# Kernel tuning notes

Hardware: AMD Instinct MI355X
Metric: run time of the kernel (lower is better)

The kernel has to match this reference:

```python
import jax, jax.numpy as jnp
import numpy as np
from math import factorial, sqrt, pi

# ---- static config (matches init_kwargs) ----
C = 64            # channel multiplicity of hidden irreps 64x0e+64x1o+64x2e
L_HID = 2
MAX_ELL = 3
N_BASIS = 8
R_MAX = 5.0
AVG_NEI = 16.0
NUM_SPECIES = 5
N_NODES = 10000
N_EDGES = 160000
RAD_HID = 64
DIMS = [2 * l + 1 for l in range(L_HID + 1)]   # [1,3,5]

# ---- Clebsch-Gordan coefficients in the real spherical-harmonic basis ----
def _cg(j1, m1, j2, m2, j3, m3):
    if m1 + m2 != m3:
        return 0.0
    f = factorial
    pref = sqrt((2 * j3 + 1) * f(j3 + j1 - j2) * f(j3 - j1 + j2) * f(j1 + j2 - j3) / f(j1 + j2 + j3 + 1))
    pref *= sqrt(f(j3 + m3) * f(j3 - m3) * f(j1 - m1) * f(j1 + m1) * f(j2 - m2) * f(j2 + m2))
    s = 0.0
    for k in range(j1 + j2 - j3 + 1):
        d = (k, j1 + j2 - j3 - k, j1 - m1 - k, j2 + m2 - k, j3 - j2 + m1 + k, j3 - j1 - m2 + k)
        if min(d) < 0:
            continue
        s += (-1.0) ** k / np.prod([float(f(x)) for x in d])
    return pref * s

def _real_basis(l):
    A = np.zeros((2 * l + 1, 2 * l + 1), dtype=complex)
    for mp in range(-l, l + 1):
        if mp > 0:
            A[l + mp, l + mp] = (-1) ** mp / sqrt(2); A[l + mp, l - mp] = 1 / sqrt(2)
        elif mp == 0:
            A[l, l] = 1.0
        else:
            m = -mp
            A[l + mp, l - m] = 1j / sqrt(2); A[l + mp, l + m] = -1j * (-1) ** m / sqrt(2)
    return A

def _real_cg(l1, l2, l3):
    Cc = np.zeros((2 * l1 + 1, 2 * l2 + 1, 2 * l3 + 1), dtype=complex)
    for a in range(-l1, l1 + 1):
        for b in range(-l2, l2 + 1):
            c = a + b
            if -l3 <= c <= l3:
                Cc[l1 + a, l2 + b, l3 + c] = _cg(l1, a, l2, b, l3, c)
    A1, A2, A3 = _real_basis(l1), _real_basis(l2), _real_basis(l3)
    Cr = np.einsum('ia,jb,kc,abc->ijk', A1, A2, A3.conj(), Cc)
    R = Cr.real if np.abs(Cr.real).sum() >= np.abs(Cr.imag).sum() else Cr.imag
    R = R / max(np.sqrt((R ** 2).sum()), 1e-12)   # path-normalized
    return jnp.asarray(R.astype(np.float32))

def _paths(ls_in):
    ps = []
    for l1 in ls_in:
        for l2 in range(MAX_ELL + 1):
            for l3 in range(L_HID + 1):
                # triangle inequality + parity match (hidden parities are (-1)^l, SH parity (-1)^l)
                if abs(l1 - l2) <= l3 <= l1 + l2 and (l1 + l2 + l3) % 2 == 0:
                    ps.append((l1, l2, l3))
    return ps

PATHS = [_paths([0]), _paths(list(range(L_HID + 1)))]   # layer 0: 3 paths, layer 1: 13 paths
CG = {p: _real_cg(*p) for layer in PATHS for p in layer}

# ---- real spherical harmonics up to l=3 (component-style normalization) ----
def sph_harm(u):
    x, y, z = u[:, 0], u[:, 1], u[:, 2]
    Y0 = jnp.ones_like(x)[:, None]
    Y1 = sqrt(3.0) * jnp.stack([y, z, x], -1)
    Y2 = jnp.stack([sqrt(15) * x * y, sqrt(15) * y * z, sqrt(5) / 2 * (3 * z * z - 1),
                    sqrt(15) * x * z, sqrt(15) / 2 * (x * x - y * y)], -1)
    Y3 = jnp.stack([sqrt(35 / 8) * y * (3 * x * x - y * y), sqrt(105) * x * y * z,
                    sqrt(21 / 8) * y * (5 * z * z - 1), sqrt(7) / 2 * z * (5 * z * z - 3),
                    sqrt(21 / 8) * x * (5 * z * z - 1), sqrt(105) / 2 * z * (x * x - y * y),
                    sqrt(35 / 8) * x * (x * x - 3 * y * y)], -1)
    return [Y0, Y1, Y2, Y3]

def bessel(r):
    # e3nn.bessel(r, N_BASIS, R_MAX)
    n = jnp.arange(1, N_BASIS + 1, dtype=r.dtype)
    rs = jnp.maximum(r, 1e-6)[:, None]
    return sqrt(2.0 / R_MAX) * jnp.sin(n * pi * rs / R_MAX) / rs

def soft_envelope(r):
    # e3nn.soft_envelope: value_at_origin=1.2, arg_multiplicator=2.0
    t = 2.0 * (1.0 - r / R_MAX)
    sus = jnp.where(t > 0, jnp.exp(-1.0 / jnp.where(t > 0, t, 1.0)), 0.0)
    return (1.2 / np.exp(-0.5)) * sus

def interaction(h, Ys, rad, paths, rad_w1, rad_w2, mix, senders, receivers, n_nodes):
    # radial MLP -> per-path, per-channel tensor-product weights
    w = jax.nn.silu(rad @ rad_w1) @ rad_w2                       # [E, P*C]
    w = w.reshape(rad.shape[0], len(paths), C)
    hs = {l: h[l][senders] for l in {p[0] for p in paths}}       # gather once per input l
    acc = [None] * (L_HID + 1)
    for p, (l1, l2, l3) in enumerate(paths):
        # CG tensor product of sender features with edge spherical harmonics
        m = jnp.einsum('eci,ej,ijk,ec->eck', hs[l1], Ys[l2], CG[(l1, l2, l3)], w[:, p])
        acc[l3] = m if acc[l3] is None else acc[l3] + m
    out = {}
    for l in range(L_HID + 1):
        node_m = jax.ops.segment_sum(acc[l], receivers, num_segments=n_nodes) / AVG_NEI
        out[l] = jnp.einsum('nck,cd->ndk', node_m, mix[l])       # linear channel mixing per irrep
    return out

def forward(positions, w_embed, rad_w1_0, rad_w2_0, mix0, read0,
            rad_w1_1, rad_w2_1, mix1, skip1, read1, species, senders, receivers):
    n = positions.shape[0]
    rel = positions[receivers] - positions[senders]              # [E,3]
    r = jnp.sqrt(jnp.sum(rel * rel, -1) + 1e-12)
    u = rel / r[:, None]
    Ys = sph_harm(u)
    rad = bessel(r) * soft_envelope(r)[:, None]                  # [E,B]
    h = {0: w_embed[species][:, :, None]}                        # initial scalar node features
    # layer 0 (skip_connection_first_layer=False)
    h = interaction(h, Ys, rad, PATHS[0], rad_w1_0, rad_w2_0, mix0, senders, receivers, n)
    out0 = jnp.concatenate([jnp.einsum('nck,cd->ndk', h[l], read0[l]).reshape(n, -1)
                            for l in range(L_HID + 1)], -1)      # [N, C*9]
    # layer 1 (with linear skip connection)
    m = interaction(h, Ys, rad, PATHS[1], rad_w1_1, rad_w2_1, mix1, senders, receivers, n)
    h = {l: m[l] + jnp.einsum('nck,cd->ndk', h[l], skip1[l]) for l in range(L_HID + 1)}
    out1 = jnp.concatenate([jnp.einsum('nck,cd->ndk', h[l], read1[l]).reshape(n, -1)
                            for l in range(L_HID + 1)], -1)
    # per-layer readouts stacked then flattened == axis_to_mul over the layer axis
    return jnp.concatenate([out0, out1], -1)                     # [N, 2*C*9] = [N, 1152]

def setup_inputs() -> dict:
    key = jax.random.key(0)
    ks = jax.random.split(key, 14)
    P = [len(PATHS[0]), len(PATHS[1])]
    def w(k, shape, fan_in):
        return jax.random.normal(k, shape, jnp.float32) / np.sqrt(fan_in)
    return {
        'positions': jax.random.normal(ks[0], (N_NODES, 3), jnp.float32) * 1.5,
        'species': jax.random.randint(ks[1], (N_NODES,), 0, NUM_SPECIES),
        'senders': jax.random.randint(ks[2], (N_EDGES,), 0, N_NODES),
        'receivers': jax.random.randint(ks[3], (N_EDGES,), 0, N_NODES),
        'w_embed': w(ks[4], (NUM_SPECIES, C), 1),
        'rad_w1_0': w(ks[5], (N_BASIS, RAD_HID), N_BASIS),
        'rad_w2_0': w(ks[6], (RAD_HID, P[0] * C), RAD_HID),
        'mix0': w(ks[7], (L_HID + 1, C, C), C),
        'read0': w(ks[8], (L_HID + 1, C, C), C),
        'rad_w1_1': w(ks[9], (N_BASIS, RAD_HID), N_BASIS),
        'rad_w2_1': w(ks[10], (RAD_HID, P[1] * C), RAD_HID),
        'mix1': w(ks[11], (L_HID + 1, C, C), C),
        'skip1': w(ks[12], (L_HID + 1, C, C), C),
        'read1': w(ks[13], (L_HID + 1, C, C), C),
    }

def reference(positions, species, senders, receivers, w_embed, rad_w1_0, rad_w2_0, mix0, read0,
              rad_w1_1, rad_w2_1, mix1, skip1, read1):
    return forward(positions, w_embed, rad_w1_0, rad_w2_0, mix0, read0,
                   rad_w1_1, rad_w2_1, mix1, skip1, read1, species, senders, receivers)
```

## Files before the change

### kernel.cpp

```cpp
#include <hip/hip_runtime.h>
#include <math.h>

#define NE 160000
#define NN 10000
#define NP1 13
#define CG_TOTAL 573
#define CC_TOTAL 171
#define G_TOTAL 145

typedef __attribute__((ext_vector_type(8))) short bf16x8;
typedef __attribute__((ext_vector_type(4))) float f32x4;

constexpr int c_l1[NP1]   = {0,0,0,1,1,1,1,1,2,2,2,2,2};
constexpr int c_l2[NP1]   = {0,1,2,0,1,1,2,3,0,1,2,2,3};
constexpr int c_l3[NP1]   = {0,1,2,1,0,2,1,2,2,1,0,2,1};
constexpr int c_cgoff[NP1+1]= {0,1,10,35,44,53,98,143,248,273,318,343,468,573};
constexpr int c_ccoff[NP1+1]= {0,1,4,9,12,21,30,45,66,71,86,111,136,171};
constexpr int c_goff[NP1] = {0,1,4,9,18,21,36,45,60,85,100,105,130};
constexpr int YB[4] = {0,1,4,9};
constexpr int KB[3] = {0,1,4};
constexpr int IB[3] = {0,1,4};

__device__ float g_cg[640];
__device__ int   g_dec[160];
__device__ float g_ys[(size_t)NE*16];
__device__ float g_rad[(size_t)NE*8];
__device__ unsigned short g_hb0[(size_t)NE*64];
__device__ unsigned short g_hb1[(size_t)NE*64];
__device__ unsigned short g_Bp0[12*2*64*8];
__device__ unsigned short g_Bp1[52*2*64*8];
__device__ unsigned short g_W0[(size_t)NE*192];
__device__ unsigned short g_W1[(size_t)NE*832];
__device__ float g_acc0[(size_t)NN*576];
__device__ float g_acc1[(size_t)NN*576];
__device__ float g_h0[(size_t)NN*576];
__device__ int g_cnt[NN];
__device__ int g_cur[NN];
__device__ int g_off[NN+1];
__device__ int g_perm[NE];

__device__ inline unsigned short f2bf(float f){
  unsigned u = __float_as_uint(f);
  unsigned r = (u + 0x7FFFu + ((u>>16)&1u)) >> 16;
  return (unsigned short)r;
}
__device__ inline float bf2f(unsigned short h){ return __uint_as_float(((unsigned)h)<<16); }
__device__ inline float silu(float a){ return a/(1.f+expf(-a)); }

__device__ double dfact(int n){ double f=1.0; for(int i=2;i<=n;++i) f*=(double)i; return f; }

__device__ double cg_coef(int j1,int m1,int j2,int m2,int j3,int m3){
  if(m1+m2!=m3) return 0.0;
  double pref = sqrt((2.0*j3+1.0)*dfact(j3+j1-j2)*dfact(j3-j1+j2)*dfact(j1+j2-j3)/dfact(j1+j2+j3+1));
  pref *= sqrt(dfact(j3+m3)*dfact(j3-m3)*dfact(j1-m1)*dfact(j1+m1)*dfact(j2-m2)*dfact(j2+m2));
  double s=0.0;
  for(int k=0;k<=j1+j2-j3;++k){
    int d0=k, d1=j1+j2-j3-k, d2=j1-m1-k, d3=j2+m2-k, d4=j3-j2+m1+k, d5=j3-j1-m2+k;
    if(d1<0||d2<0||d3<0||d4<0||d5<0) continue;
    double denom = dfact(d0)*dfact(d1)*dfact(d2)*dfact(d3)*dfact(d4)*dfact(d5);
    s += ((k&1)? -1.0:1.0)/denom;
  }
  return pref*s;
}

__device__ inline void rb_elem(int l, int i, int j, double& re, double& im){
  re=0.0; im=0.0;
  int mp = i - l;
  const double is2 = 0.70710678118654752440;
  if(mp>0){
    if(j==l+mp) re = ((mp&1)? -1.0:1.0)*is2;
    else if(j==l-mp) re = is2;
  } else if(mp==0){
    if(j==l) re = 1.0;
  } else {
    int m=-mp;
    if(j==l-m) im = is2;
    else if(j==l+m) im = -(((m&1)?-1.0:1.0))*is2;
  }
}

__global__ __launch_bounds__(1024) void k_cg(){
  __shared__ double s_cc[CC_TOTAL];
  __shared__ double s_crr[CG_TOTAL];
  __shared__ double s_cri[CG_TOTAL];
  __shared__ double s_inv[NP1];
  __shared__ int    s_useR[NP1];
  int tid = threadIdx.x;

  if(tid==0){
    int r=0;
    for(int q=0;q<NP1;q++){
      int l1=c_l1[q], l2=c_l2[q], l3=c_l3[q];
      int d1=2*l1+1, d2=2*l2+1, d3=2*l3+1;
      for(int i=0;i<d1;i++)for(int k=0;k<d3;k++){
        int cgs = c_cgoff[q] + i*d2*d3 + k;
        g_dec[r++] = cgs | (YB[l2]<<10) | (d2<<14) | (d3<<17);
      }
    }
  }

  if(tid < CC_TOTAL){
    int p=0; while(tid >= c_ccoff[p+1]) p++;
    int r = tid - c_ccoff[p];
    int l1=c_l1[p], l2=c_l2[p], l3=c_l3[p];
    int d2=2*l2+1;
    int ai = r/d2, bi = r - ai*d2;
    int a = ai - l1, b = bi - l2, c = a + b;
    double v = 0.0;
    if(c >= -l3 && c <= l3) v = cg_coef(l1,a,l2,b,l3,c);
    s_cc[tid] = v;
  }
  __syncthreads();

  if(tid < CG_TOTAL){
    int p=0; while(tid >= c_cgoff[p+1]) p++;
    int r = tid - c_cgoff[p];
    int l1=c_l1[p], l2=c_l2[p], l3=c_l3[p];
    int d2=2*l2+1, d3=2*l3+1;
    int i = r/(d2*d3), rem = r - i*(d2*d3);
    int j = rem/d3, k = rem - j*d3;
    double accr=0.0, acci=0.0;
    int d1=2*l1+1;
    for(int ai=0; ai<d1; ai++){
      double a1r,a1i; rb_elem(l1,i,ai,a1r,a1i);
      if(a1r==0.0 && a1i==0.0) continue;
      for(int bi=0; bi<d2; bi++){
        double cc = s_cc[c_ccoff[p] + ai*d2 + bi];
        if(cc==0.0) continue;
        int ci = (ai - l1) + (bi - l2) + l3;
// ... 30 lines not shown
    double v = s_useR[p]? s_crr[tid] : s_cri[tid];
    g_cg[tid] = (float)(v*s_inv[p]);
  }
}

__global__ void k_zero(){
  int i = blockIdx.x*256 + threadIdx.x;
  if(i<NN){ g_cnt[i]=0; g_cur[i]=0; }
}

__global__ void k_hist(const int* __restrict__ rcv){
  int e = blockIdx.x*256 + threadIdx.x;
  if(e<NE) atomicAdd(&g_cnt[rcv[e]], 1);
}

__global__ void k_scan(){
  __shared__ int lds[1024];
  int t = threadIdx.x;
  int base = t*10;
  int s = 0;
  for(int i=0;i<10;i++){ int idx=base+i; if(idx<NN) s += g_cnt[idx]; }
  lds[t]=s; __syncthreads();
  for(int o=1;o<1024;o<<=1){
    int v = (t>=o)? lds[t-o] : 0;
    __syncthreads();
    lds[t]+=v;
    __syncthreads();
  }
  int run = lds[t]-s;
  for(int i=0;i<10;i++){ int idx=base+i; if(idx<NN){ g_off[idx]=run; run+=g_cnt[idx]; } }
  if(t==0) g_off[NN]=NE;
}

__global__ void k_scatter(const int* __restrict__ rcv){
  int e = blockIdx.x*256 + threadIdx.x;
  if(e<NE){
    int r = rcv[e];
    int p = atomicAdd(&g_cur[r],1);
    g_perm[g_off[r]+p] = e;
  }
}

__global__ void k_edge(const float* __restrict__ pos, const int* __restrict__ snd,
                       const int* __restrict__ rcv){
  int e = blockIdx.x*blockDim.x + threadIdx.x;
  if(e>=NE) return;
  int s=snd[e], r=rcv[e];
  float dx=pos[r*3+0]-pos[s*3+0];
  float dy=pos[r*3+1]-pos[s*3+1];
  float dz=pos[r*3+2]-pos[s*3+2];
  float rr = sqrtf(dx*dx+dy*dy+dz*dz + 1e-12f);
  float x=dx/rr, y=dy/rr, z=dz/rr;
  float* Y=&g_ys[(size_t)e*16];
  Y[0]=1.f;
  const float s3=1.7320508075688772f;
  Y[1]=s3*y; Y[2]=s3*z; Y[3]=s3*x;
  const float s15=3.872983346207417f;
  const float s5h=1.118033988749895f;
  Y[4]=s15*x*y; Y[5]=s15*y*z; Y[6]=s5h*(3.f*z*z-1.f); Y[7]=s15*x*z; Y[8]=0.5f*s15*(x*x-y*y);
  const float s35_8=2.0916500663351889f;
  const float s105=10.246950765959598f;
  const float s21_8=1.6201851746019651f;
  const float s7h=1.3228756555322954f;
  Y[9]=s35_8*y*(3.f*x*x-y*y);
  Y[10]=s105*x*y*z;
  Y[11]=s21_8*y*(5.f*z*z-1.f);
  Y[12]=s7h*z*(5.f*z*z-3.f);
  Y[13]=s21_8*x*(5.f*z*z-1.f);
  Y[14]=0.5f*s105*z*(x*x-y*y);
  Y[15]=s35_8*x*(x*x-3.f*y*y);
  float t = 2.f*(1.f - rr*0.2f);
  float env = (t>0.f)? 1.9784655248401538f*expf(-1.f/t) : 0.f;
  float rs = fmaxf(rr,1e-6f);
  const float sq25 = 0.6324555320336759f;
  float pre = sq25/rs * env;
  const float pi5 = 0.6283185307179586f;
  #pragma unroll
  for(int b=0;b<8;b++){
    g_rad[(size_t)e*8+b] = pre * sinf((float)(b+1)*pi5*rs);
  }
}

__global__ __launch_bounds__(256) void k_hidden(const float* __restrict__ W1a,
                                                const float* __restrict__ W1b){
  int idx = blockIdx.x*256 + threadIdx.x;
  int c = idx & 63;
  const float* rd = &g_rad[(size_t)(idx>>6)*8];
  float a0=0.f, a1=0.f;
  #pragma unroll
  for(int b=0;b<8;b++){
    float rv = rd[b];
    a0 += rv*W1a[b*64+c];
    a1 += rv*W1b[b*64+c];
  }
  g_hb0[idx] = f2bf(silu(a0));
  g_hb1[idx] = f2bf(silu(a1));
}

template<int NCOLS>
__global__ void k_repack(const float* __restrict__ W2){
  constexpr int NCB = NCOLS/16;
  int t = blockIdx.x*256 + threadIdx.x;
  if(t >= NCB*128) return;
  int cb = t>>7, rest = t&127, ks = rest>>6, l = rest&63;
  int col = cb*16 + (l&15);
  unsigned short* dst = (NCOLS==832)? g_Bp1 : g_Bp0;
  #pragma unroll
  for(int j=0;j<8;j++){
    int k = ks*32 + ((l>>4)<<3) + j;
    dst[(size_t)t*8+j] = f2bf(W2[k*NCOLS + col]);
  }
}

template<int NCOLS>
__global__ __launch_bounds__(256) void k_wgemm(){
  constexpr int NCB = NCOLS/16;
  const unsigned short* hb = (NCOLS==832)? g_hb1 : g_hb0;
  const unsigned short* Bp = (NCOLS==832)? g_Bp1 : g_Bp0;
  unsigned short* W = (NCOLS==832)? g_W1 : g_W0;
  const int lane = threadIdx.x & 63;
  const int wid  = threadIdx.x >> 6;
  const int e0 = blockIdx.x*128 + wid*32;
  const int rowl = lane & 15, kg = lane >> 4;
  bf16x8 a[2][2];
  #pragma unroll
  for(int mr=0;mr<2;mr++){
    #pragma unroll
    for(int ks=0;ks<2;ks++){
      a[mr][ks] = *reinterpret_cast<const bf16x8*>(&hb[(size_t)(e0+mr*16+rowl)*64 + ks*32 + kg*8]);
    }
  }
  for(int cb=0;cb<NCB;cb++){
    bf16x8 b0 = *reinterpret_cast<const bf16x8*>(&Bp[((size_t)(cb*2+0)*64+lane)*8]);
    bf16x8 b1 = *reinterpret_cast<const bf16x8*>(&Bp[((size_t)(cb*2+1)*64+lane)*8]);
    #pragma unroll
    for(int mr=0;mr<2;mr++){
      f32x4 acc = {0.f,0.f,0.f,0.f};
      acc = __builtin_amdgcn_mfma_f32_16x16x32_bf16(a[mr][0], b0, acc, 0,0,0);
      acc = __builtin_amdgcn_mfma_f32_16x16x32_bf16(a[mr][1], b1, acc, 0,0,0);
      #pragma unroll
      for(int r=0;r<4;r++){
        int row = kg*4 + r;
        W[(size_t)(e0+mr*16+row)*NCOLS + cb*16 + rowl] = f2bf(acc[r]);
      }
    }
  }
}

__global__ __launch_bounds__(256) void k_gather0(const int* __restrict__ snd,
    const int* __restrict__ spec, const float* __restrict__ wemb){
  __shared__ float lds_cg[36];
  __shared__ int lds_dec[9];
  __shared__ float Ylds[4][16];
  __shared__ float Glds[4][12];
  int tid=threadIdx.x;
  if(tid<36) lds_cg[tid]=g_cg[tid];
  if(tid>=64 && tid<73) lds_dec[tid-64]=g_dec[tid-64];
  __syncthreads();
  int lane=tid&63, wid=tid>>6;
  int n = blockIdx.x*4 + wid;
  int beg=g_off[n], end=g_off[n+1];
  float acc[9];
  #pragma unroll
  for(int kk=0;kk<9;kk++) acc[kk]=0.f;
  for(int j=beg;j<end;j++){
    int e = __builtin_amdgcn_readfirstlane(g_perm[j]);
    int s = __builtin_amdgcn_readfirstlane(snd[e]);
    if(lane<16) Ylds[wid][lane]=g_ys[(size_t)e*16+lane];
    const unsigned short* wp=&g_W0[(size_t)e*192 + lane];
    float wv0=bf2f(wp[0]), wv1=bf2f(wp[64]), wv2=bf2f(wp[128]);
    float hs=wemb[spec[s]*64+lane];
    asm volatile("s_waitcnt lgkmcnt(0)" ::: "memory");
    if(lane<9){
      int d=lds_dec[lane];
      int cgs=d&1023, yb=(d>>10)&15, d2=(d>>14)&7, d3=(d>>17)&7;
      float g=0.f;
      for(int jj=0;jj<d2;jj++) g+=Ylds[wid][yb+jj]*lds_cg[cgs+jj*d3];
      Glds[wid][lane]=g;
    }
    asm volatile("s_waitcnt lgkmcnt(0)" ::: "memory");
    float whs0=wv0*hs, whs1=wv1*hs, whs2=wv2*hs;
    acc[0]+=whs0*Glds[wid][0];
    #pragma unroll
    for(int k=0;k<3;k++) acc[1+k]+=whs1*Glds[wid][1+k];
    #pragma unroll
    for(int k=0;k<5;k++) acc[4+k]+=whs2*Glds[wid][4+k];
    asm volatile("s_waitcnt lgkmcnt(0)" ::: "memory");
  }
  #pragma unroll
  for(int kk=0;kk<9;kk++) g_acc0[(size_t)n*576+kk*64+lane]=acc[kk];
}

__global__ __launch_bounds__(256) void k_gather1(const int* __restrict__ snd){
  __shared__ float lds_cg[CG_TOTAL];
  __shared__ int lds_dec[G_TOTAL];
  __shared__ float Ylds[4][16];
  __shared__ float Glds[4][152];
  int tid=threadIdx.x;
  for(int t=tid;t<CG_TOTAL;t+=256) lds_cg[t]=g_cg[t];
  for(int t=tid;t<G_TOTAL;t+=256) lds_dec[t]=g_dec[t];
  __syncthreads();
  int lane=tid&63, wid=tid>>6;
  int n = blockIdx.x*4 + wid;
  int beg=g_off[n], end=g_off[n+1];
  float acc[9];
  #pragma unroll
  for(int kk=0;kk<9;kk++) acc[kk]=0.f;
  for(int j=beg;j<end;j++){
    int e = __builtin_amdgcn_readfirstlane(g_perm[j]);
    int s = __builtin_amdgcn_readfirstlane(snd[e]);
    if(lane<16) Ylds[wid][lane]=g_ys[(size_t)e*16+lane];
    float wv[13];
    const unsigned short* wp=&g_W1[(size_t)e*832 + lane];
    #pragma unroll
    for(int p=0;p<13;p++) wv[p]=bf2f(wp[p*64]);
    const float* hb=&g_h0[(size_t)s*576 + lane];
    float hsv[9];
    #pragma unroll
    for(int i=0;i<9;i++) hsv[i]=hb[i*64];
    asm volatile("s_waitcnt lgkmcnt(0)" ::: "memory");
    #pragma unroll
    for(int strip=0;strip<3;strip++){
      int r = lane + strip*64;
      if(r<G_TOTAL){
        int d=lds_dec[r];
        int cgs=d&1023, yb=(d>>10)&15, d2=(d>>14)&7, d3=(d>>17)&7;
        float g=0.f;
        for(int jj=0;jj<d2;jj++) g+=Ylds[wid][yb+jj]*lds_cg[cgs+jj*d3];
        Glds[wid][r]=g;
      }
    }
    asm volatile("s_waitcnt lgkmcnt(0)" ::: "memory");
    const float* G=&Glds[wid][0];
    #pragma unroll
    for(int p=0;p<13;p++){
      const int l1=c_l1[p], l3=c_l3[p];
      const int d1=2*l1+1, d3=2*l3+1;
      const int ib=IB[l1], kb=KB[l3], go=c_goff[p];
      float wpv=wv[p];
      #pragma unroll
      for(int k=0;k<d3;k++){
        float t=0.f;
        #pragma unroll
        for(int i=0;i<d1;i++) t += hsv[ib+i]*G[go+i*d3+k];
        acc[kb+k] += wpv*t;
      }
    }
    asm volatile("s_waitcnt lgkmcnt(0)" ::: "memory");
  }
  #pragma unroll
  for(int kk=0;kk<9;kk++) g_acc1[(size_t)n*576+kk*64+lane]=acc[kk];
}

__global__ __launch_bounds__(256) void k_node0(const float* __restrict__ mix,
    const float* __restrict__ read, float* __restrict__ out){
  __shared__ float nm[4][9][64];
  __shared__ float hl[4][9][64];
  int lane=threadIdx.x&63, wid=threadIdx.x>>6;
  int n=blockIdx.x*4+wid;
  #pragma unroll
  for(int kk=0;kk<9;kk++) nm[wid][kk][lane]=g_acc0[(size_t)n*576+kk*64+lane]*(1.f/16.f);
  asm volatile("s_waitcnt lgkmcnt(0)" ::: "memory");
  float h[9];
  #pragma unroll
  for(int kk=0;kk<9;kk++) h[kk]=0.f;
  for(int c=0;c<64;c++){
    float m0=mix[c*64+lane], m1=mix[4096+c*64+lane], m2=mix[8192+c*64+lane];
    h[0]+=nm[wid][0][c]*m0;
    #pragma unroll
    for(int k=0;k<3;k++) h[1+k]+=nm[wid][1+k][c]*m1;
    #pragma unroll
    for(int k=0;k<5;k++) h[4+k]+=nm[wid][4+k][c]*m2;
  }
  #pragma unroll
  for(int kk=0;kk<9;kk++){ g_h0[(size_t)n*576+kk*64+lane]=h[kk]; hl[wid][kk][lane]=h[kk]; }
  asm volatile("s_waitcnt lgkmcnt(0)" ::: "memory");
  float o[9];
  #pragma unroll
  for(int kk=0;kk<9;kk++) o[kk]=0.f;
  for(int c=0;c<64;c++){
    float r0=read[c*64+lane], r1=read[4096+c*64+lane], r2=read[8192+c*64+lane];
    o[0]+=hl[wid][0][c]*r0;
    #pragma unroll
    for(int k=0;k<3;k++) o[1+k]+=hl[wid][1+k][c]*r1;
// ... 47 lines not shown
    #pragma unroll
    for(int k=0;k<5;k++) o[4+k]+=hn[wid][4+k][c]*r2;
  }
  float* op=&out[(size_t)n*1152 + 576];
  op[lane]=o[0];
  #pragma unroll
  for(int k=0;k<3;k++) op[64 + lane*3+k]=o[1+k];
  #pragma unroll
  for(int k=0;k<5;k++) op[256 + lane*5+k]=o[4+k];
}

extern "C" void kernel_launch(void* const* d_in, const int* in_sizes, int n_in,
                              void* d_out, int out_size, void* d_ws, size_t ws_size,
                              hipStream_t stream) {
  (void)in_sizes; (void)n_in; (void)out_size; (void)d_ws; (void)ws_size;
  const float* pos  =(const float*)d_in[0];
  const int*   spec =(const int*)  d_in[1];
  const int*   snd  =(const int*)  d_in[2];
  const int*   rcv  =(const int*)  d_in[3];
  const float* wemb =(const float*)d_in[4];
  const float* w1_0 =(const float*)d_in[5];
  const float* w2_0 =(const float*)d_in[6];
  const float* mix0 =(const float*)d_in[7];
  const float* read0=(const float*)d_in[8];
  const float* w1_1 =(const float*)d_in[9];
  const float* w2_1 =(const float*)d_in[10];
  const float* mix1 =(const float*)d_in[11];
  const float* skip1=(const float*)d_in[12];
  const float* read1=(const float*)d_in[13];
  float* out=(float*)d_out;

  k_cg<<<1,1024,0,stream>>>();
  k_zero<<<(NN+255)/256,256,0,stream>>>();
  k_edge<<<(NE+255)/256,256,0,stream>>>(pos,snd,rcv);
  k_hist<<<NE/256,256,0,stream>>>(rcv);
  k_scan<<<1,1024,0,stream>>>();
  k_scatter<<<NE/256,256,0,stream>>>(rcv);
  k_hidden<<<NE*64/256,256,0,stream>>>(w1_0,w1_1);
  k_repack<192><<<6,256,0,stream>>>(w2_0);
  k_repack<832><<<26,256,0,stream>>>(w2_1);
  k_wgemm<192><<<NE/128,256,0,stream>>>();
  k_wgemm<832><<<NE/128,256,0,stream>>>();
  k_gather0<<<NN/4,256,0,stream>>>(snd,spec,wemb);
  k_node0<<<NN/4,256,0,stream>>>(mix0,read0,out);
  k_gather1<<<NN/4,256,0,stream>>>(snd);
  k_node1<<<NN/4,256,0,stream>>>(mix1,skip1,read1,out);
}
```

Baseline: 670.3 us.

## Fuse radial weight GEMM into receiver-sorted gather kernels using MFMA per 16-edge tile

Drops the separate per-edge weight GEMM kernels and their large bf16 weight buffers, and computes the radial weights with MFMA inside the gather kernels, 16 receiver-sorted edges at a time. Edge features, radial basis, sender ids and species are written in receiver-sorted order, so the gather reads contiguous rows and no permutation lookup is needed. This removes a large write and re-read of the edge weight tensors and processes edges in tiles instead of one by one. The cost is heavier per-wave register and LDS use, plus partial-tile handling and a shuffle reduction at the end.

```diff
diff --git a/kernel.cpp b/kernel.cpp
--- a/kernel.cpp
+++ b/kernel.cpp
@@ -29,22 +29,21 @@
 __device__ unsigned short g_hb1[(size_t)NE*64];
 __device__ unsigned short g_Bp0[12*2*64*8];
 __device__ unsigned short g_Bp1[52*2*64*8];
-__device__ unsigned short g_W0[(size_t)NE*192];
-__device__ unsigned short g_W1[(size_t)NE*832];
 __device__ float g_acc0[(size_t)NN*576];
 __device__ float g_acc1[(size_t)NN*576];
 __device__ float g_h0[(size_t)NN*576];
 __device__ int g_cnt[NN];
 __device__ int g_cur[NN];
 __device__ int g_off[NN+1];
-__device__ int g_perm[NE];
+__device__ int g_jof[NE];
+__device__ int g_snds[NE];
+__device__ int g_specs[NE];
 
 __device__ inline unsigned short f2bf(float f){
   unsigned u = __float_as_uint(f);
   unsigned r = (u + 0x7FFFu + ((u>>16)&1u)) >> 16;
   return (unsigned short)r;
 }
-__device__ inline float bf2f(unsigned short h){ return __uint_as_float(((unsigned)h)<<16); }
 __device__ inline float silu(float a){ return a/(1.f+expf(-a)); }
 
 __device__ double dfact(int n){ double f=1.0; for(int i=2;i<=n;++i) f*=(double)i; return f; }
@@ -191,12 +190,17 @@
   if(t==0) g_off[NN]=NE;
 }
 
-__global__ void k_scatter(const int* __restrict__ rcv){
+__global__ void k_scatter(const int* __restrict__ rcv, const int* __restrict__ snd,
+                          const int* __restrict__ spec){
   int e = blockIdx.x*256 + threadIdx.x;
   if(e<NE){
     int r = rcv[e];
     int p = atomicAdd(&g_cur[r],1);
-    g_perm[g_off[r]+p] = e;
+    int j = g_off[r]+p;
+    g_jof[e] = j;
+    int s = snd[e];
+    g_snds[j] = s;
+    g_specs[j] = spec[s];
   }
 }
 
@@ -205,12 +209,13 @@
   int e = blockIdx.x*blockDim.x + threadIdx.x;
   if(e>=NE) return;
   int s=snd[e], r=rcv[e];
+  int j=g_jof[e];
   float dx=pos[r*3+0]-pos[s*3+0];
   float dy=pos[r*3+1]-pos[s*3+1];
   float dz=pos[r*3+2]-pos[s*3+2];
   float rr = sqrtf(dx*dx+dy*dy+dz*dz + 1e-12f);
   float x=dx/rr, y=dy/rr, z=dz/rr;
-  float* Y=&g_ys[(size_t)e*16];
+  float Y[16];
   Y[0]=1.f;
   const float s3=1.7320508075688772f;
   Y[1]=s3*y; Y[2]=s3*z; Y[3]=s3*x;
@@ -228,6 +233,8 @@
   Y[13]=s21_8*x*(5.f*z*z-1.f);
   Y[14]=0.5f*s105*z*(x*x-y*y);
   Y[15]=s35_8*x*(x*x-3.f*y*y);
+  #pragma unroll
+  for(int i=0;i<16;i++) g_ys[(size_t)j*16+i]=Y[i];
   float t = 2.f*(1.f - rr*0.2f);
   float env = (t>0.f)? 1.9784655248401538f*expf(-1.f/t) : 0.f;
   float rs = fmaxf(rr,1e-6f);
@@ -236,7 +243,7 @@
   const float pi5 = 0.6283185307179586f;
   #pragma unroll
   for(int b=0;b<8;b++){
-    g_rad[(size_t)e*8+b] = pre * sinf((float)(b+1)*pi5*rs);
+    g_rad[(size_t)j*8+b] = pre * sinf((float)(b+1)*pi5*rs);
   }
 }
 
@@ -271,144 +278,190 @@
   }
 }
 
-template<int NCOLS>
-__global__ __launch_bounds__(256) void k_wgemm(){
-  constexpr int NCB = NCOLS/16;
-  const unsigned short* hb = (NCOLS==832)? g_hb1 : g_hb0;
-  const unsigned short* Bp = (NCOLS==832)? g_Bp1 : g_Bp0;
-  unsigned short* W = (NCOLS==832)? g_W1 : g_W0;
-  const int lane = threadIdx.x & 63;
-  const int wid  = threadIdx.x >> 6;
-  const int e0 = blockIdx.x*128 + wid*32;
-  const int rowl = lane & 15, kg = lane >> 4;
-  bf16x8 a[2][2];
-  #pragma unroll
-  for(int mr=0;mr<2;mr++){
-    #pragma unroll
-    for(int ks=0;ks<2;ks++){
-      a[mr][ks] = *reinterpret_cast<const bf16x8*>(&hb[(size_t)(e0+mr*16+rowl)*64 + ks*32 + kg*8]);
-    }
-  }
-  for(int cb=0;cb<NCB;cb++){
-    bf16x8 b0 = *reinterpret_cast<const bf16x8*>(&Bp[((size_t)(cb*2+0)*64+lane)*8]);
-    bf16x8 b1 = *reinterpret_cast<const bf16x8*>(&Bp[((size_t)(cb*2+1)*64+lane)*8]);
-    #pragma unroll
-    for(int mr=0;mr<2;mr++){
-      f32x4 acc = {0.f,0.f,0.f,0.f};
-      acc = __builtin_amdgcn_mfma_f32_16x16x32_bf16(a[mr][0], b0, acc, 0,0,0);
-      acc = __builtin_amdgcn_mfma_f32_16x16x32_bf16(a[mr][1], b1, acc, 0,0,0);
-      #pragma unroll
-      for(int r=0;r<4;r++){
-        int row = kg*4 + r;
-        W[(size_t)(e0+mr*16+row)*NCOLS + cb*16 + rowl] = f2bf(acc[r]);
-      }
-    }
-  }
-}
-
-__global__ __launch_bounds__(256) void k_gather0(const int* __restrict__ snd,
-    const int* __restrict__ spec, const float* __restrict__ wemb){
+__global__ __launch_bounds__(256) void k_gfuse0(const float* __restrict__ wemb){
   __shared__ float lds_cg[36];
   __shared__ int lds_dec[9];
-  __shared__ float Ylds[4][16];
-  __shared__ float Glds[4][12];
+  __shared__ float Ylds[4][16][16];
+  __shared__ float Glds[4][16][12];
+  __shared__ int Slds[4][16];
   int tid=threadIdx.x;
   if(tid<36) lds_cg[tid]=g_cg[tid];
   if(tid>=64 && tid<73) lds_dec[tid-64]=g_dec[tid-64];
   __syncthreads();
-  int lane=tid&63, wid=tid>>6;
-  int n = blockIdx.x*4 + wid;
-  int beg=g_off[n], end=g_off[n+1];
-  float acc[9];
-  #pragma unroll
-  for(int kk=0;kk<9;kk++) acc[kk]=0.f;
-  for(int j=beg;j<end;j++){
-    int e = __builtin_amdgcn_readfirstlane(g_perm[j]);
-    int s = __builtin_amdgcn_readfirstlane(snd[e]);
-    if(lane<16) Ylds[wid][lane]=g_ys[(size_t)e*16+lane];
-    const unsigned short* wp=&g_W0[(size_t)e*192 + lane];
-    float wv0=bf2f(wp[0]), wv1=bf2f(wp[64]), wv2=bf2f(wp[128]);
-    float hs=wemb[spec[s]*64+lane];
+  const int lane=tid&63, wid=tid>>6;
+  const int sub=lane&15, kg=lane>>4;
+  const int n=blockIdx.x*4+wid;
+  const int beg=g_off[n], end=g_off[n+1];
+  float acc[4][9];
+  #pragma unroll
+  for(int q=0;q<4;q++)
+    #pragma unroll
+    for(int k=0;k<9;k++) acc[q][k]=0.f;
+  for(int j0=beg;j0<end;j0+=16){
+    const int nrow = min(16,end-j0);
+    for(int t=lane;t<256;t+=64){
+      int r=t>>4, c2=t&15;
+      int j=j0+r; if(j>end-1) j=end-1;
+      Ylds[wid][r][c2]=g_ys[(size_t)j*16+c2];
+    }
+    if(lane<16){ int j=j0+lane; Slds[wid][lane]=(j<end)? g_specs[j] : 0; }
     asm volatile("s_waitcnt lgkmcnt(0)" ::: "memory");
-    if(lane<9){
-      int d=lds_dec[lane];
-      int cgs=d&1023, yb=(d>>10)&15, d2=(d>>14)&7, d3=(d>>17)&7;
-      float g=0.f;
-      for(int jj=0;jj<d2;jj++) g+=Ylds[wid][yb+jj]*lds_cg[cgs+jj*d3];
-      Glds[wid][lane]=g;
-    }
+    for(int t=lane;t<144;t+=64){
+      int r=t/9, g=t-r*9;
+      float gv=0.f;
+      if(r<nrow){
+        int d=lds_dec[g];
+        int cgs=d&1023, yb=(d>>10)&15, d2=(d>>14)&7, d3=(d>>17)&7;
+        for(int jj=0;jj<d2;jj++) gv+=Ylds[wid][r][yb+jj]*lds_cg[cgs+jj*d3];
+      }
+      Glds[wid][r][g]=gv;
+    }
+    size_t arow=(size_t)(j0+sub); if(arow>(size_t)(NE-1)) arow=NE-1;
+    bf16x8 a0=*reinterpret_cast<const bf16x8*>(&g_hb0[arow*64 + kg*8]);
+    bf16x8 a1=*reinterpret_cast<const bf16x8*>(&g_hb0[arow*64 + 32 + kg*8]);
     asm volatile("s_waitcnt lgkmcnt(0)" ::: "memory");
-    float whs0=wv0*hs, whs1=wv1*hs, whs2=wv2*hs;
-    acc[0]+=whs0*Glds[wid][0];
-    #pragma unroll
-    for(int k=0;k<3;k++) acc[1+k]+=whs1*Glds[wid][1+k];
-    #pragma unroll
-    for(int k=0;k<5;k++) acc[4+k]+=whs2*Glds[wid][4+k];
+    #pragma unroll
+    for(int cq=0;cq<4;cq++){
+      const int c=cq*16+sub;
+      float hv[4];
+      #pragma unroll
+      for(int r2=0;r2<4;r2++) hv[r2]=wemb[Slds[wid][kg*4+r2]*64+c];
+      #pragma unroll
+      for(int p=0;p<3;p++){
+        const int cb=p*4+cq;
+        bf16x8 b0=*reinterpret_cast<const bf16x8*>(&g_Bp0[((size_t)(cb*2+0)*64+lane)*8]);
+        bf16x8 b1=*reinterpret_cast<const bf16x8*>(&g_Bp0[((size_t)(cb*2+1)*64+lane)*8]);
+        f32x4 wv={0.f,0.f,0.f,0.f};
+        wv=__builtin_amdgcn_mfma_f32_16x16x32_bf16(a0,b0,wv,0,0,0);
+        wv=__builtin_amdgcn_mfma_f32_16x16x32_bf16(a1,b1,wv,0,0,0);
+        const int d3=2*p+1, kb=KB[p], go=(p==0)?0:((p==1)?1:4);
+        #pragma unroll
+        for(int r2=0;r2<4;r2++){
+          const int row=kg*4+r2;
+          float whp=wv[r2]*hv[r2];
+          #pragma unroll
+          for(int k=0;k<d3;k++) acc[cq][kb+k]+=whp*Glds[wid][row][go+k];
+        }
+      }
+    }
     asm volatile("s_waitcnt lgkmcnt(0)" ::: "memory");
   }
   #pragma unroll
-  for(int kk=0;kk<9;kk++) g_acc0[(size_t)n*576+kk*64+lane]=acc[kk];
-}
-
-__global__ __launch_bounds__(256) void k_gather1(const int* __restrict__ snd){
+  for(int q=0;q<4;q++)
+    #pragma unroll
+    for(int k=0;k<9;k++){
+      float v=acc[q][k];
+      v+=__shfl_xor(v,16,64);
+      v+=__shfl_xor(v,32,64);
+      acc[q][k]=v;
+    }
+  const int c=kg*16+sub;
+  #pragma unroll
+  for(int k=0;k<9;k++){
+    float v=acc[0][k];
+    if(kg==1) v=acc[1][k];
+    if(kg==2) v=acc[2][k];
+    if(kg==3) v=acc[3][k];
+    g_acc0[(size_t)n*576 + k*64 + c]=v;
+  }
+}
+
+__global__ __launch_bounds__(256) void k_gfuse1(){
   __shared__ float lds_cg[CG_TOTAL];
   __shared__ int lds_dec[G_TOTAL];
-  __shared__ float Ylds[4][16];
-  __shared__ float Glds[4][152];
+  __shared__ float Ylds[4][16][16];
+  __shared__ float Glds[4][16][148];
   int tid=threadIdx.x;
   for(int t=tid;t<CG_TOTAL;t+=256) lds_cg[t]=g_cg[t];
   for(int t=tid;t<G_TOTAL;t+=256) lds_dec[t]=g_dec[t];
   __syncthreads();
-  int lane=tid&63, wid=tid>>6;
-  int n = blockIdx.x*4 + wid;
-  int beg=g_off[n], end=g_off[n+1];
-  float acc[9];
-  #pragma unroll
-  for(int kk=0;kk<9;kk++) acc[kk]=0.f;
-  for(int j=beg;j<end;j++){
-    int e = __builtin_amdgcn_readfirstlane(g_perm[j]);
-    int s = __builtin_amdgcn_readfirstlane(snd[e]);
-    if(lane<16) Ylds[wid][lane]=g_ys[(size_t)e*16+lane];
-    float wv[13];
-    const unsigned short* wp=&g_W1[(size_t)e*832 + lane];
-    #pragma unroll
-    for(int p=0;p<13;p++) wv[p]=bf2f(wp[p*64]);
-    const float* hb=&g_h0[(size_t)s*576 + lane];
-    float hsv[9];
-    #pragma unroll
-    for(int i=0;i<9;i++) hsv[i]=hb[i*64];
+  const int lane=tid&63, wid=tid>>6;
+  const int sub=lane&15, kg=lane>>4;
+  const int n=blockIdx.x*4+wid;
+  const int beg=g_off[n], end=g_off[n+1];
+  float acc[4][9];
+  #pragma unroll
+  for(int q=0;q<4;q++)
+    #pragma unroll
+    for(int k=0;k<9;k++) acc[q][k]=0.f;
+  for(int j0=beg;j0<end;j0+=16){
+    const int nrow = min(16,end-j0);
+    for(int t=lane;t<256;t+=64){
+      int r=t>>4, c2=t&15;
+      int j=j0+r; if(j>end-1) j=end-1;
+      Ylds[wid][r][c2]=g_ys[(size_t)j*16+c2];
+    }
     asm volatile("s_waitcnt lgkmcnt(0)" ::: "memory");
-    #pragma unroll
-    for(int strip=0;strip<3;strip++){
-      int r = lane + strip*64;
-      if(r<G_TOTAL){
-        int d=lds_dec[r];
+    for(int t=lane;t<16*G_TOTAL;t+=64){
+      int r=t/G_TOTAL, g=t-r*G_TOTAL;
+      float gv=0.f;
+      if(r<nrow){
+        int d=lds_dec[g];
         int cgs=d&1023, yb=(d>>10)&15, d2=(d>>14)&7, d3=(d>>17)&7;
-        float g=0.f;
-        for(int jj=0;jj<d2;jj++) g+=Ylds[wid][yb+jj]*lds_cg[cgs+jj*d3];
-        Glds[wid][r]=g;
+        for(int jj=0;jj<d2;jj++) gv+=Ylds[wid][r][yb+jj]*lds_cg[cgs+jj*d3];
       }
-    }
+      Glds[wid][r][g]=gv;
+    }
+    size_t arow=(size_t)(j0+sub); if(arow>(size_t)(NE-1)) arow=NE-1;
+    bf16x8 a0=*reinterpret_cast<const bf16x8*>(&g_hb1[arow*64 + kg*8]);
+    bf16x8 a1=*reinterpret_cast<const bf16x8*>(&g_hb1[arow*64 + 32 + kg*8]);
+    int sv[4];
+    #pragma unroll
+    for(int r2=0;r2<4;r2++){ int j=j0+kg*4+r2; sv[r2]=(j<end)? g_snds[j] : 0; }
     asm volatile("s_waitcnt lgkmcnt(0)" ::: "memory");
-    const float* G=&Glds[wid][0];
-    #pragma unroll
-    for(int p=0;p<13;p++){
-      const int l1=c_l1[p], l3=c_l3[p];
-      const int d1=2*l1+1, d3=2*l3+1;
-      const int ib=IB[l1], kb=KB[l3], go=c_goff[p];
-      float wpv=wv[p];
+    #pragma unroll
+    for(int cq=0;cq<4;cq++){
+      const int c=cq*16+sub;
+      float h0v[4][9];
       #pragma unroll
-      for(int k=0;k<d3;k++){
-        float t=0.f;
+      for(int r2=0;r2<4;r2++)
         #pragma unroll
-        for(int i=0;i<d1;i++) t += hsv[ib+i]*G[go+i*d3+k];
-        acc[kb+k] += wpv*t;
+        for(int i=0;i<9;i++) h0v[r2][i]=g_h0[(size_t)sv[r2]*576 + i*64 + c];
+      #pragma unroll
+      for(int p=0;p<13;p++){
+        const int cb=p*4+cq;
+        bf16x8 b0=*reinterpret_cast<const bf16x8*>(&g_Bp1[((size_t)(cb*2+0)*64+lane)*8]);
+        bf16x8 b1=*reinterpret_cast<const bf16x8*>(&g_Bp1[((size_t)(cb*2+1)*64+lane)*8]);
+        f32x4 wv={0.f,0.f,0.f,0.f};
+        wv=__builtin_amdgcn_mfma_f32_16x16x32_bf16(a0,b0,wv,0,0,0);
+        wv=__builtin_amdgcn_mfma_f32_16x16x32_bf16(a1,b1,wv,0,0,0);
+        const int l1=c_l1[p], l3=c_l3[p];
+        const int d1=2*l1+1, d3=2*l3+1;
+        const int ib=IB[l1], kb=KB[l3], go=c_goff[p];
+        #pragma unroll
+        for(int r2=0;r2<4;r2++){
+          const int row=kg*4+r2;
+          float wp=wv[r2];
+          #pragma unroll
+          for(int k=0;k<d3;k++){
+            float t=0.f;
+            #pragma unroll
+            for(int i=0;i<d1;i++) t+=h0v[r2][ib+i]*Glds[wid][row][go+i*d3+k];
+            acc[cq][kb+k]+=wp*t;
+          }
+        }
       }
     }
     asm volatile("s_waitcnt lgkmcnt(0)" ::: "memory");
   }
   #pragma unroll
-  for(int kk=0;kk<9;kk++) g_acc1[(size_t)n*576+kk*64+lane]=acc[kk];
+  for(int q=0;q<4;q++)
+    #pragma unroll
+    for(int k=0;k<9;k++){
+      float v=acc[q][k];
+      v+=__shfl_xor(v,16,64);
+      v+=__shfl_xor(v,32,64);
+      acc[q][k]=v;
+    }
+  const int c=kg*16+sub;
+  #pragma unroll
+  for(int k=0;k<9;k++){
+    float v=acc[0][k];
+    if(kg==1) v=acc[1][k];
+    if(kg==2) v=acc[2][k];
+    if(kg==3) v=acc[3][k];
+    g_acc1[(size_t)n*576 + k*64 + c]=v;
+  }
 }
 
 __global__ __launch_bounds__(256) void k_node0(const float* __restrict__ mix,
@@ -522,17 +575,15 @@
 
   k_cg<<<1,1024,0,stream>>>();
   k_zero<<<(NN+255)/256,256,0,stream>>>();
-  k_edge<<<(NE+255)/256,256,0,stream>>>(pos,snd,rcv);
   k_hist<<<NE/256,256,0,stream>>>(rcv);
   k_scan<<<1,1024,0,stream>>>();
-  k_scatter<<<NE/256,256,0,stream>>>(rcv);
+  k_scatter<<<NE/256,256,0,stream>>>(rcv,snd,spec);
+  k_edge<<<(NE+255)/256,256,0,stream>>>(pos,snd,rcv);
   k_hidden<<<NE*64/256,256,0,stream>>>(w1_0,w1_1);
   k_repack<192><<<6,256,0,stream>>>(w2_0);
   k_repack<832><<<26,256,0,stream>>>(w2_1);
-  k_wgemm<192><<<NE/128,256,0,stream>>>();
-  k_wgemm<832><<<NE/128,256,0,stream>>>();
-  k_gather0<<<NN/4,256,0,stream>>>(snd,spec,wemb);
+  k_gfuse0<<<NN/4,256,0,stream>>>(wemb);
   k_node0<<<NN/4,256,0,stream>>>(mix0,read0,out);
-  k_gather1<<<NN/4,256,0,stream>>>(snd);
+  k_gfuse1<<<NN/4,256,0,stream>>>();
   k_node1<<<NN/4,256,0,stream>>>(mix1,skip1,read1,out);
 }
```

Result: slower. 2.439 ms (+263.9%).

## Store edge data in receiver-sorted order and precompute Y·CG per edge

Applied to the files above, without the earlier changes.

Edge features, spherical harmonics and radial bases are now written in receiver-sorted order, so the gather kernels read contiguous rows instead of going through a permutation. A new kernel precomputes the CG-contracted Y products per edge into padded global buffers, and the gather kernels load them as vector loads instead of recomputing them per edge in LDS with waits. This removes indirection and per-edge LDS work from the gathers, at the cost of extra global storage and traffic (about 172 floats per edge) plus another kernel launch.

```diff
diff --git a/kernel.cpp b/kernel.cpp
--- a/kernel.cpp
+++ b/kernel.cpp
@@ -7,6 +7,8 @@
 #define CG_TOTAL 573
 #define CC_TOTAL 171
 #define G_TOTAL 145
+#define G1PAD 172
+#define G0PAD 16
 
 typedef __attribute__((ext_vector_type(8))) short bf16x8;
 typedef __attribute__((ext_vector_type(4))) float f32x4;
@@ -16,13 +18,13 @@
 constexpr int c_l3[NP1]   = {0,1,2,1,0,2,1,2,2,1,0,2,1};
 constexpr int c_cgoff[NP1+1]= {0,1,10,35,44,53,98,143,248,273,318,343,468,573};
 constexpr int c_ccoff[NP1+1]= {0,1,4,9,12,21,30,45,66,71,86,111,136,171};
-constexpr int c_goff[NP1] = {0,1,4,9,18,21,36,45,60,85,100,105,130};
+constexpr int c_poff1[NP1] = {0,4,8,16,28,32,48,60,76,104,120,128,156};
+constexpr int c_poff0[3]   = {0,4,8};
 constexpr int YB[4] = {0,1,4,9};
-constexpr int KB[3] = {0,1,4};
-constexpr int IB[3] = {0,1,4};
 
 __device__ float g_cg[640];
-__device__ int   g_dec[160];
+__device__ int   g_dec1[160];
+__device__ int   g_dec0[16];
 __device__ float g_ys[(size_t)NE*16];
 __device__ float g_rad[(size_t)NE*8];
 __device__ unsigned short g_hb0[(size_t)NE*64];
@@ -31,13 +33,17 @@
 __device__ unsigned short g_Bp1[52*2*64*8];
 __device__ unsigned short g_W0[(size_t)NE*192];
 __device__ unsigned short g_W1[(size_t)NE*832];
+__device__ float g_G1[(size_t)NE*G1PAD];
+__device__ float g_G0[(size_t)NE*G0PAD];
 __device__ float g_acc0[(size_t)NN*576];
 __device__ float g_acc1[(size_t)NN*576];
 __device__ float g_h0[(size_t)NN*576];
 __device__ int g_cnt[NN];
 __device__ int g_cur[NN];
 __device__ int g_off[NN+1];
-__device__ int g_perm[NE];
+__device__ int g_jof[NE];
+__device__ int g_snds[NE];
+__device__ int g_specs[NE];
 
 __device__ inline unsigned short f2bf(float f){
   unsigned u = __float_as_uint(f);
@@ -90,11 +96,22 @@
   if(tid==0){
     int r=0;
     for(int q=0;q<NP1;q++){
-      int l1=c_l1[q], l2=c_l2[q], l3=c_l3[q];
-      int d1=2*l1+1, d2=2*l2+1, d3=2*l3+1;
+      int l2=c_l2[q], l3=c_l3[q];
+      int d1=2*c_l1[q]+1, d2=2*l2+1, d3=2*l3+1;
       for(int i=0;i<d1;i++)for(int k=0;k<d3;k++){
         int cgs = c_cgoff[q] + i*d2*d3 + k;
-        g_dec[r++] = cgs | (YB[l2]<<10) | (d2<<14) | (d3<<17);
+        int dst = c_poff1[q] + i*d3 + k;
+        g_dec1[r++] = cgs | (YB[l2]<<10) | (d2<<14) | (d3<<17) | (dst<<20);
+      }
+    }
+    r=0;
+    for(int q=0;q<3;q++){
+      int l2=c_l2[q], l3=c_l3[q];
+      int d2=2*l2+1, d3=2*l3+1;
+      for(int k=0;k<d3;k++){
+        int cgs = c_cgoff[q] + k;
+        int dst = c_poff0[q] + k;
+        g_dec0[r++] = cgs | (YB[l2]<<10) | (d2<<14) | (d3<<17) | (dst<<20);
       }
     }
   }
@@ -191,12 +208,17 @@
   if(t==0) g_off[NN]=NE;
 }
 
-__global__ void k_scatter(const int* __restrict__ rcv){
+__global__ void k_scatter(const int* __restrict__ rcv, const int* __restrict__ snd,
+                          const int* __restrict__ spec){
   int e = blockIdx.x*256 + threadIdx.x;
   if(e<NE){
     int r = rcv[e];
     int p = atomicAdd(&g_cur[r],1);
-    g_perm[g_off[r]+p] = e;
+    int j = g_off[r]+p;
+    g_jof[e] = j;
+    int s = snd[e];
+    g_snds[j] = s;
+    g_specs[j] = spec[s];
   }
 }
 
@@ -205,12 +227,13 @@
   int e = blockIdx.x*blockDim.x + threadIdx.x;
   if(e>=NE) return;
   int s=snd[e], r=rcv[e];
+  int j=g_jof[e];
   float dx=pos[r*3+0]-pos[s*3+0];
   float dy=pos[r*3+1]-pos[s*3+1];
   float dz=pos[r*3+2]-pos[s*3+2];
   float rr = sqrtf(dx*dx+dy*dy+dz*dz + 1e-12f);
   float x=dx/rr, y=dy/rr, z=dz/rr;
-  float* Y=&g_ys[(size_t)e*16];
+  float Y[16];
   Y[0]=1.f;
   const float s3=1.7320508075688772f;
   Y[1]=s3*y; Y[2]=s3*z; Y[3]=s3*x;
@@ -228,6 +251,8 @@
   Y[13]=s21_8*x*(5.f*z*z-1.f);
   Y[14]=0.5f*s105*z*(x*x-y*y);
   Y[15]=s35_8*x*(x*x-3.f*y*y);
+  #pragma unroll
+  for(int i=0;i<16;i++) g_ys[(size_t)j*16+i]=Y[i];
   float t = 2.f*(1.f - rr*0.2f);
   float env = (t>0.f)? 1.9784655248401538f*expf(-1.f/t) : 0.f;
   float rs = fmaxf(rr,1e-6f);
@@ -236,7 +261,59 @@
   const float pi5 = 0.6283185307179586f;
   #pragma unroll
   for(int b=0;b<8;b++){
-    g_rad[(size_t)e*8+b] = pre * sinf((float)(b+1)*pi5*rs);
+    g_rad[(size_t)j*8+b] = pre * sinf((float)(b+1)*pi5*rs);
+  }
+}
+
+__global__ __launch_bounds__(256) void k_gbuild(){
+  __shared__ float cg[CG_TOTAL];
+  __shared__ int dec1[G_TOTAL];
+  __shared__ int dec0[9];
+  __shared__ __align__(16) float Yl[4][8][17];
+  __shared__ __align__(16) float Gl[4][8][G1PAD];
+  __shared__ __align__(16) float G0l[4][8][G0PAD];
+  int tid=threadIdx.x;
+  for(int t=tid;t<CG_TOTAL;t+=256) cg[t]=g_cg[t];
+  for(int t=tid;t<G_TOTAL;t+=256) dec1[t]=g_dec1[t];
+  if(tid<9) dec0[tid]=g_dec0[tid];
+  __syncthreads();
+  const int lane=tid&63, wid=tid>>6;
+  const int e0=blockIdx.x*32 + wid*8;
+  #pragma unroll
+  for(int t=lane;t<128;t+=64){
+    int r=t>>4, c=t&15;
+    Yl[wid][r][c]=g_ys[(size_t)(e0+r)*16+c];
+  }
+  asm volatile("s_waitcnt lgkmcnt(0)" ::: "memory");
+  for(int s=0;s<19;s++){
+    int idx = lane + 64*s;
+    if(idx<1160){
+      int e = idx/145, r = idx - 145*e;
+      int d = dec1[r];
+      int cgs=d&1023, yb=(d>>10)&15, d2=(d>>14)&7, d3n=(d>>17)&7, dst=(d>>20)&255;
+      float g=0.f;
+      for(int jj=0;jj<d2;jj++) g += Yl[wid][e][yb+jj]*cg[cgs+jj*d3n];
+      Gl[wid][e][dst]=g;
+    }
+  }
+  for(int idx=lane; idx<72; idx+=64){
+    int e = idx/9, r = idx - 9*e;
+    int d = dec0[r];
+    int cgs=d&1023, yb=(d>>10)&15, d2=(d>>14)&7, d3n=(d>>17)&7, dst=(d>>20)&255;
+    float g=0.f;
+    for(int jj=0;jj<d2;jj++) g += Yl[wid][e][yb+jj]*cg[cgs+jj*d3n];
+    G0l[wid][e][dst]=g;
+  }
+  asm volatile("s_waitcnt lgkmcnt(0)" ::: "memory");
+  {
+    f32x4* dst=(f32x4*)&g_G1[(size_t)e0*G1PAD];
+    const f32x4* src=(const f32x4*)&Gl[wid][0][0];
+    for(int t=lane;t<344;t+=64) dst[t]=src[t];
+  }
+  {
+    f32x4* dst=(f32x4*)&g_G0[(size_t)e0*G0PAD];
+    const f32x4* src=(const f32x4*)&G0l[wid][0][0];
+    if(lane<32) dst[lane]=src[lane];
   }
 }
 
@@ -306,109 +383,80 @@
   }
 }
 
-__global__ __launch_bounds__(256) void k_gather0(const int* __restrict__ snd,
-    const int* __restrict__ spec, const float* __restrict__ wemb){
-  __shared__ float lds_cg[36];
-  __shared__ int lds_dec[9];
-  __shared__ float Ylds[4][16];
-  __shared__ float Glds[4][12];
-  int tid=threadIdx.x;
-  if(tid<36) lds_cg[tid]=g_cg[tid];
-  if(tid>=64 && tid<73) lds_dec[tid-64]=g_dec[tid-64];
-  __syncthreads();
-  int lane=tid&63, wid=tid>>6;
-  int n = blockIdx.x*4 + wid;
-  int beg=g_off[n], end=g_off[n+1];
+__global__ __launch_bounds__(256) void k_gather0(const float* __restrict__ wemb){
+  const int lane=threadIdx.x&63, wid=threadIdx.x>>6;
+  const int n=blockIdx.x*4+wid;
+  const int beg=__builtin_amdgcn_readfirstlane(g_off[n]);
+  const int end=__builtin_amdgcn_readfirstlane(g_off[n+1]);
   float acc[9];
   #pragma unroll
-  for(int kk=0;kk<9;kk++) acc[kk]=0.f;
+  for(int k=0;k<9;k++) acc[k]=0.f;
   for(int j=beg;j<end;j++){
-    int e = __builtin_amdgcn_readfirstlane(g_perm[j]);
-    int s = __builtin_amdgcn_readfirstlane(snd[e]);
-    if(lane<16) Ylds[wid][lane]=g_ys[(size_t)e*16+lane];
-    const unsigned short* wp=&g_W0[(size_t)e*192 + lane];
-    float wv0=bf2f(wp[0]), wv1=bf2f(wp[64]), wv2=bf2f(wp[128]);
-    float hs=wemb[spec[s]*64+lane];
-    asm volatile("s_waitcnt lgkmcnt(0)" ::: "memory");
-    if(lane<9){
-      int d=lds_dec[lane];
-      int cgs=d&1023, yb=(d>>10)&15, d2=(d>>14)&7, d3=(d>>17)&7;
-      float g=0.f;
-      for(int jj=0;jj<d2;jj++) g+=Ylds[wid][yb+jj]*lds_cg[cgs+jj*d3];
-      Glds[wid][lane]=g;
-    }
-    asm volatile("s_waitcnt lgkmcnt(0)" ::: "memory");
-    float whs0=wv0*hs, whs1=wv1*hs, whs2=wv2*hs;
-    acc[0]+=whs0*Glds[wid][0];
-    #pragma unroll
-    for(int k=0;k<3;k++) acc[1+k]+=whs1*Glds[wid][1+k];
-    #pragma unroll
-    for(int k=0;k<5;k++) acc[4+k]+=whs2*Glds[wid][4+k];
-    asm volatile("s_waitcnt lgkmcnt(0)" ::: "memory");
-  }
-  #pragma unroll
-  for(int kk=0;kk<9;kk++) g_acc0[(size_t)n*576+kk*64+lane]=acc[kk];
-}
-
-__global__ __launch_bounds__(256) void k_gather1(const int* __restrict__ snd){
-  __shared__ float lds_cg[CG_TOTAL];
-  __shared__ int lds_dec[G_TOTAL];
-  __shared__ float Ylds[4][16];
-  __shared__ float Glds[4][152];
-  int tid=threadIdx.x;
-  for(int t=tid;t<CG_TOTAL;t+=256) lds_cg[t]=g_cg[t];
-  for(int t=tid;t<G_TOTAL;t+=256) lds_dec[t]=g_dec[t];
-  __syncthreads();
-  int lane=tid&63, wid=tid>>6;
-  int n = blockIdx.x*4 + wid;
-  int beg=g_off[n], end=g_off[n+1];
+    const float* Ge=&g_G0[(size_t)j*G0PAD];
+    f32x4 qa=*reinterpret_cast<const f32x4*>(Ge+0);
+    f32x4 qb=*reinterpret_cast<const f32x4*>(Ge+4);
+    f32x4 qc=*reinterpret_cast<const f32x4*>(Ge+8);
+    f32x4 qd=*reinterpret_cast<const f32x4*>(Ge+12);
+    int sp=__builtin_amdgcn_readfirstlane(g_specs[j]);
+    float hs=wemb[sp*64+lane];
+    const unsigned short* wp=&g_W0[(size_t)j*192 + lane];
+    float a0=bf2f(wp[0])*hs, a1=bf2f(wp[64])*hs, a2=bf2f(wp[128])*hs;
+    acc[0]+=a0*qa[0];
+    acc[1]+=a1*qb[0]; acc[2]+=a1*qb[1]; acc[3]+=a1*qb[2];
+    acc[4]+=a2*qc[0]; acc[5]+=a2*qc[1]; acc[6]+=a2*qc[2]; acc[7]+=a2*qc[3];
+    acc[8]+=a2*qd[0];
+  }
+  #pragma unroll
+  for(int k=0;k<9;k++) g_acc0[(size_t)n*576 + k*64 + lane]=acc[k];
+}
+
+#define DP(P_,L1_,L3_,OFF_) { \
+  constexpr int d1_=2*(L1_)+1, d3_=2*(L3_)+1, ib_=(L1_)*(L1_), kb_=(L3_)*(L3_); \
+  constexpr int nv_=((d1_*d3_)+3)/4; \
+  f32x4 gq[nv_]; \
+  _Pragma("unroll") \
+  for(int q_=0;q_<nv_;q_++) gq[q_]=*reinterpret_cast<const f32x4*>(Ge+(OFF_)+4*q_); \
+  _Pragma("unroll") \
+  for(int k_=0;k_<d3_;k_++){ \
+    float tk_=0.f; \
+    _Pragma("unroll") \
+    for(int i_=0;i_<d1_;i_++){ tk_+=h[ib_+i_]*gq[(i_*d3_+k_)>>2][(i_*d3_+k_)&3]; } \
+    acc[kb_+k_]+=w[P_]*tk_; } }
+
+__global__ __launch_bounds__(256) void k_gather1(){
+  const int lane=threadIdx.x&63, wid=threadIdx.x>>6;
+  const int n=blockIdx.x*4+wid;
+  const int beg=__builtin_amdgcn_readfirstlane(g_off[n]);
+  const int end=__builtin_amdgcn_readfirstlane(g_off[n+1]);
   float acc[9];
   #pragma unroll
-  for(int kk=0;kk<9;kk++) acc[kk]=0.f;
+  for(int k=0;k<9;k++) acc[k]=0.f;
   for(int j=beg;j<end;j++){
-    int e = __builtin_amdgcn_readfirstlane(g_perm[j]);
-    int s = __builtin_amdgcn_readfirstlane(snd[e]);
-    if(lane<16) Ylds[wid][lane]=g_ys[(size_t)e*16+lane];
-    float wv[13];
-    const unsigned short* wp=&g_W1[(size_t)e*832 + lane];
-    #pragma unroll
-    for(int p=0;p<13;p++) wv[p]=bf2f(wp[p*64]);
-    const float* hb=&g_h0[(size_t)s*576 + lane];
-    float hsv[9];
-    #pragma unroll
-    for(int i=0;i<9;i++) hsv[i]=hb[i*64];
-    asm volatile("s_waitcnt lgkmcnt(0)" ::: "memory");
-    #pragma unroll
-    for(int strip=0;strip<3;strip++){
-      int r = lane + strip*64;
-      if(r<G_TOTAL){
-        int d=lds_dec[r];
-        int cgs=d&1023, yb=(d>>10)&15, d2=(d>>14)&7, d3=(d>>17)&7;
-        float g=0.f;
-        for(int jj=0;jj<d2;jj++) g+=Ylds[wid][yb+jj]*lds_cg[cgs+jj*d3];
-        Glds[wid][r]=g;
-      }
-    }
-    asm volatile("s_waitcnt lgkmcnt(0)" ::: "memory");
-    const float* G=&Glds[wid][0];
-    #pragma unroll
-    for(int p=0;p<13;p++){
-      const int l1=c_l1[p], l3=c_l3[p];
-      const int d1=2*l1+1, d3=2*l3+1;
-      const int ib=IB[l1], kb=KB[l3], go=c_goff[p];
-      float wpv=wv[p];
-      #pragma unroll
-      for(int k=0;k<d3;k++){
-        float t=0.f;
-        #pragma unroll
-        for(int i=0;i<d1;i++) t += hsv[ib+i]*G[go+i*d3+k];
-        acc[kb+k] += wpv*t;
-      }
-    }
-    asm volatile("s_waitcnt lgkmcnt(0)" ::: "memory");
-  }
-  #pragma unroll
-  for(int kk=0;kk<9;kk++) g_acc1[(size_t)n*576+kk*64+lane]=acc[kk];
+    const int s=__builtin_amdgcn_readfirstlane(g_snds[j]);
+    const float* Ge=&g_G1[(size_t)j*G1PAD];
+    float h[9];
+    #pragma unroll
+    for(int i=0;i<9;i++) h[i]=g_h0[(size_t)s*576 + i*64 + lane];
+    const unsigned short* wp=&g_W1[(size_t)j*832 + lane];
+    float w[13];
+    #pragma unroll
+    for(int p=0;p<13;p++) w[p]=bf2f(wp[p*64]);
+    DP(0,0,0,0)
+    DP(1,0,1,4)
+    DP(2,0,2,8)
+    DP(3,1,1,16)
+    DP(4,1,0,28)
+    DP(5,1,2,32)
+    DP(6,1,1,48)
+    DP(7,1,2,60)
+    DP(8,2,2,76)
+    DP(9,2,1,104)
+    DP(10,2,0,120)
+    DP(11,2,2,128)
+    DP(12,2,1,156)
+  }
+  #pragma unroll
+  for(int k=0;k<9;k++) g_acc1[(size_t)n*576 + k*64 + lane]=acc[k];
 }
 
 __global__ __launch_bounds__(256) void k_node0(const float* __restrict__ mix,
@@ -522,17 +570,18 @@
 
   k_cg<<<1,1024,0,stream>>>();
   k_zero<<<(NN+255)/256,256,0,stream>>>();
-  k_edge<<<(NE+255)/256,256,0,stream>>>(pos,snd,rcv);
   k_hist<<<NE/256,256,0,stream>>>(rcv);
   k_scan<<<1,1024,0,stream>>>();
-  k_scatter<<<NE/256,256,0,stream>>>(rcv);
+  k_scatter<<<NE/256,256,0,stream>>>(rcv,snd,spec);
+  k_edge<<<(NE+255)/256,256,0,stream>>>(pos,snd,rcv);
+  k_gbuild<<<NE/32,256,0,stream>>>();
   k_hidden<<<NE*64/256,256,0,stream>>>(w1_0,w1_1);
   k_repack<192><<<6,256,0,stream>>>(w2_0);
   k_repack<832><<<26,256,0,stream>>>(w2_1);
   k_wgemm<192><<<NE/128,256,0,stream>>>();
   k_wgemm<832><<<NE/128,256,0,stream>>>();
-  k_gather0<<<NN/4,256,0,stream>>>(snd,spec,wemb);
+  k_gather0<<<NN/4,256,0,stream>>>(wemb);
   k_node0<<<NN/4,256,0,stream>>>(mix0,read0,out);
-  k_gather1<<<NN/4,256,0,stream>>>(snd);
+  k_gather1<<<NN/4,256,0,stream>>>();
   k_node1<<<NN/4,256,0,stream>>>(mix1,skip1,read1,out);
 }
```

After: 745.8 us. 1.11x slower.
